# Performance work log

Measured on AMD Instinct MI355X. Metric: run time of the kernel, lower is better.

## Reference

```python
import jax, jax.numpy as jnp
import numpy as np

NUM_HEADS = 16
WINDOW = 64


def setup_inputs() -> dict:
    key = jax.random.key(0)
    ks = jax.random.split(key, 6)
    b, l, d = 2, 2048, 1024
    s = 1.0 / np.sqrt(d)
    return {
        "x": jax.random.normal(ks[0], (b, l, d), dtype=jnp.float32),
        "Wq": jax.random.normal(ks[1], (d, d), dtype=jnp.float32) * s,
        "Wk": jax.random.normal(ks[2], (d, d), dtype=jnp.float32) * s,
        "Wv": jax.random.normal(ks[3], (d, d), dtype=jnp.float32) * s,
        "Wo": jax.random.normal(ks[4], (d, d), dtype=jnp.float32) * s,
        "bo": jax.random.normal(ks[5], (d,), dtype=jnp.float32) * 0.01,
    }


def reference(x, Wq, Wk, Wv, Wo, bo):
    b, l, d = x.shape
    h, w = NUM_HEADS, WINDOW
    dh = d // h
    p = w // 2
    # Projections. Padding is zeros and proj_k/proj_v have no bias, so
    # padding-then-projecting equals projecting-then-zero-padding.
    q = (x @ Wq.T).reshape(b, l, h, dh)                     # (b,l,h,dh)
    xp = jnp.pad(x, ((0, 0), (p, p), (0, 0)))               # (b,l+2p,d)
    k = (xp @ Wk.T).reshape(b, l + 2 * p, h, dh)
    v = (xp @ Wv.T).reshape(b, l + 2 * p, h, dh)
    # Sliding windows: query i attends to padded positions i .. i+w-1
    win_idx = jnp.arange(l)[:, None] + jnp.arange(w)[None, :]  # (l,w)
    kw = k[:, win_idx]                                       # (b,l,w,h,dh)
    vw = v[:, win_idx]                                       # (b,l,w,h,dh)
    scale = 1.0 / np.float32(np.sqrt(dh))
    scores = jnp.einsum('blhd,blwhd->blhw', q, kw) * scale   # (b,l,h,w)
    attn = jax.nn.softmax(scores, axis=-1)
    out = jnp.einsum('blhw,blwhd->blhd', attn, vw).reshape(b, l, d)
    return out @ Wo.T + bo
```

## Files before the change

kernel.cpp:

```cpp
#include <hip/hip_runtime.h>
#include <hip/hip_bf16.h>
#include <cstdint>

typedef __bf16 bf16;
typedef __bf16 bf16x4 __attribute__((ext_vector_type(4)));
typedef __bf16 bf16x8 __attribute__((ext_vector_type(8)));
typedef float floatx4 __attribute__((ext_vector_type(4)));
typedef float floatx16 __attribute__((ext_vector_type(16)));

typedef __attribute__((address_space(1))) void as1_void;
typedef __attribute__((address_space(3))) void as3_void;

__device__ __forceinline__ void gld16(const void* g, void* l) {
#if __has_builtin(__builtin_amdgcn_global_load_lds)
  __builtin_amdgcn_global_load_lds((as1_void*)(uintptr_t)g, (as3_void*)l, 16, 0, 0);
#else
  *(uint4*)l = *(const uint4*)g;
#endif
}

__global__ __launch_bounds__(256) void convert_kernel(
    const float* __restrict__ x, const float* __restrict__ wq,
    const float* __restrict__ wk, const float* __restrict__ wv,
    const float* __restrict__ wo, bf16* __restrict__ xbf,
    bf16* __restrict__ wqkv, bf16* __restrict__ wob) {
  int i = blockIdx.x * 256 + threadIdx.x;
  const float* src;
  bf16* dst;
  int off;
  if (i < 1048576) {
    src = x; dst = xbf; off = i;
  } else if (i < 1310720) {
    src = wq; dst = wqkv; off = i - 1048576;
  } else if (i < 1572864) {
    src = wk; dst = wqkv + 1048576; off = i - 1310720;
  } else if (i < 1835008) {
    src = wv; dst = wqkv + 2097152; off = i - 1572864;
  } else {
    src = wo; dst = wob; off = i - 1835008;
  }
  float4 v = ((const float4*)src)[off];
  bf16x4 o;
  o[0] = (bf16)v.x; o[1] = (bf16)v.y; o[2] = (bf16)v.z; o[3] = (bf16)v.w;
  ((bf16x4*)dst)[off] = o;
}

template <int MODE, int BM, int BN>
__global__ __launch_bounds__(256) void gemm_nt(const bf16* __restrict__ A,
                                               const bf16* __restrict__ Bm,
                                               bf16* __restrict__ Cb,
                                               float* __restrict__ Cf,
                                               const float* __restrict__ bias,
                                               int M, int N, int K) {
  constexpr int WM = BM / 2, WN = BN / 2;
  constexpr int MI = WM / 32, NI = WN / 32;
  __shared__ __attribute__((aligned(16))) bf16 As[BM * 32];
  __shared__ __attribute__((aligned(16))) bf16 Bs[BN * 32];
  const int tid = threadIdx.x;
  const int lane = tid & 63;
  const int wave = tid >> 6;
  const int m32 = lane & 31;
  const int half = lane >> 5;
  const int wm = wave >> 1;
  const int wn = wave & 1;
  const int bN = blockIdx.x, bM = blockIdx.y;
  const bf16* Ab = A + (size_t)bM * BM * K;
  const bf16* Bb = Bm + (size_t)bN * BN * K;
  floatx16 acc[MI][NI] = {};
  for (int k0 = 0; k0 < K; k0 += 32) {
#pragma unroll
    for (int cc = 0; cc < BM * 4; cc += 256) {
      const int c = cc + tid;
      gld16(Ab + (size_t)(c >> 2) * K + k0 + (c & 3) * 8, &As[c * 8]);
    }
#pragma unroll
    for (int cc = 0; cc < BN * 4; cc += 256) {
      const int c = cc + tid;
      gld16(Bb + (size_t)(c >> 2) * K + k0 + (c & 3) * 8, &Bs[c * 8]);
    }
    __syncthreads();
#pragma unroll
    for (int ks = 0; ks < 2; ++ks) {
      bf16x8 af[MI], bfr[NI];
#pragma unroll
      for (int mi = 0; mi < MI; ++mi)
        af[mi] = *(const bf16x8*)&As[(wm * WM + mi * 32 + m32) * 32 + ks * 16 + half * 8];
#pragma unroll
      for (int ni = 0; ni < NI; ++ni)
        bfr[ni] = *(const bf16x8*)&Bs[(wn * WN + ni * 32 + m32) * 32 + ks * 16 + half * 8];
#pragma unroll
      for (int mi = 0; mi < MI; ++mi)
#pragma unroll
        for (int ni = 0; ni < NI; ++ni)
          acc[mi][ni] = __builtin_amdgcn_mfma_f32_32x32x16_bf16(
              af[mi], bfr[ni], acc[mi][ni], 0, 0, 0);
    }
    __syncthreads();
  }
  const int rowBase = bM * BM + wm * WM + half * 4;
  const int colBase = bN * BN + wn * WN + m32;
#pragma unroll
  for (int ni = 0; ni < NI; ++ni) {
    const int col = colBase + ni * 32;
    float badd = 0.f;
    if (MODE == 1) badd = bias[col];
#pragma unroll
    for (int mi = 0; mi < MI; ++mi)
#pragma unroll
      for (int r = 0; r < 16; ++r) {
        const int row = rowBase + mi * 32 + (r & 3) + 8 * (r >> 2);
        if (MODE == 0)
          Cb[(size_t)row * N + col] = (bf16)acc[mi][ni][r];
        else
          Cf[(size_t)row * N + col] = acc[mi][ni][r] + badd;
      }
  }
}

__global__ __launch_bounds__(256) void attn_kernel(const bf16* __restrict__ qkv,
                                                   bf16* __restrict__ aout) {
  __shared__ __attribute__((aligned(16))) bf16 Ks[128 * 72];
  __shared__ __attribute__((aligned(16))) bf16 VsPs[128 * 72];
  __shared__ __attribute__((aligned(16))) bf16 Vt[64 * 136];
  const int bid = blockIdx.x;
  const int b = bid >> 9;
  const int h = (bid >> 5) & 15;
  const int i0 = (bid & 31) * 64;
  const int tid = threadIdx.x;
  const int wave = tid >> 6, lane = tid & 63;
  const int quad = lane >> 4, n0 = lane & 15;
  bf16* Vs = VsPs;

#pragma unroll
  for (int it = 0; it < 4; ++it) {
    const int idx = it * 256 + tid;
    const int r = idx >> 3, c = idx & 7;
    const int j = i0 - 32 + r;
    uint4 kv_ = make_uint4(0u, 0u, 0u, 0u);
    uint4 vv = make_uint4(0u, 0u, 0u, 0u);
    if (j >= 0 && j < 2048) {
      const bf16* base = qkv + (size_t)(b * 2048 + j) * 3072 + 1024 + h * 64 + c * 8;
      kv_ = *(const uint4*)base;
      vv = *(const uint4*)(base + 1024);
    }
    *(uint4*)&Ks[r * 72 + c * 8] = kv_;
    *(uint4*)&Vs[r * 72 + c * 8] = vv;
  }
  __syncthreads();

#pragma unroll
  for (int it = 0; it < 4; ++it) {
    const int idx = it * 256 + tid;
    const int t = idx & 127, c = idx >> 7;
    bf16x8 v = *(const bf16x8*)&Vs[t * 72 + c * 8];
#pragma unroll
    for (int jj = 0; jj < 8; ++jj) Vt[(c * 8 + jj) * 136 + t] = v[jj];
  }
  __syncthreads();

  bf16x8 aq[2];
#pragma unroll
  for (int ks = 0; ks < 2; ++ks)
    aq[ks] = *(const bf16x8*)(qkv +
        (size_t)(b * 2048 + i0 + wave * 16 + n0) * 3072 + h * 64 + ks * 32 + quad * 8);

  floatx4 accS[8] = {};
#pragma unroll
  for (int nt = 0; nt < 8; ++nt)
#pragma unroll
    for (int ks = 0; ks < 2; ++ks) {
      bf16x8 bk = *(const bf16x8*)&Ks[(nt * 16 + n0) * 72 + ks * 32 + quad * 8];
      accS[nt] = __builtin_amdgcn_mfma_f32_16x16x32_bf16(aq[ks], bk, accS[nt], 0, 0, 0);
    }

  float mrow[4] = {-1e30f, -1e30f, -1e30f, -1e30f};
#pragma unroll
  for (int nt = 0; nt < 8; ++nt)
#pragma unroll
    for (int r = 0; r < 4; ++r) {
      const int q64 = wave * 16 + quad * 4 + r;
      const int t = nt * 16 + n0;
      float s = accS[nt][r] * 0.125f;
      if (t < q64 || t >= q64 + 64) s = -1e30f;
      accS[nt][r] = s;
      mrow[r] = fmaxf(mrow[r], s);
    }
#pragma unroll
  for (int off = 1; off < 16; off <<= 1)
#pragma unroll
    for (int r = 0; r < 4; ++r)
      mrow[r] = fmaxf(mrow[r], __shfl_xor(mrow[r], off));
  float lrow[4] = {0.f, 0.f, 0.f, 0.f};
#pragma unroll
  for (int nt = 0; nt < 8; ++nt)
#pragma unroll
    for (int r = 0; r < 4; ++r) {
      const float e = __expf(accS[nt][r] - mrow[r]);
      accS[nt][r] = e;
      lrow[r] += e;
    }
#pragma unroll
  for (int off = 1; off < 16; off <<= 1)
#pragma unroll
    for (int r = 0; r < 4; ++r) lrow[r] += __shfl_xor(lrow[r], off);

  bf16* Pw = &VsPs[wave * 16 * 136];
#pragma unroll
  for (int r = 0; r < 4; ++r) {
    const float inv = 1.f / lrow[r];
#pragma unroll
    for (int nt = 0; nt < 8; ++nt)
      Pw[(quad * 4 + r) * 136 + nt * 16 + n0] = (bf16)(accS[nt][r] * inv);
  }

  floatx4 accO[4] = {};
#pragma unroll
  for (int kt = 0; kt < 4; ++kt) {
    bf16x8 ap = *(const bf16x8*)&Pw[n0 * 136 + kt * 32 + quad * 8];
#pragma unroll
    for (int dt = 0; dt < 4; ++dt) {
      bf16x8 bv = *(const bf16x8*)&Vt[(dt * 16 + n0) * 136 + kt * 32 + quad * 8];
      accO[dt] = __builtin_amdgcn_mfma_f32_16x16x32_bf16(ap, bv, accO[dt], 0, 0, 0);
    }
  }
#pragma unroll
  for (int dt = 0; dt < 4; ++dt)
#pragma unroll
    for (int r = 0; r < 4; ++r) {
      const int q64 = wave * 16 + quad * 4 + r;
      aout[(size_t)(b * 2048 + i0 + q64) * 1024 + h * 64 + dt * 16 + n0] =
          (bf16)accO[dt][r];
    }
}

extern "C" void kernel_launch(void* const* d_in, const int* in_sizes, int n_in,
                              void* d_out, int out_size, void* d_ws, size_t ws_size,
                              hipStream_t stream) {
  const float* x = (const float*)d_in[0];
  const float* wq = (const float*)d_in[1];
  const float* wk = (const float*)d_in[2];
  const float* wv = (const float*)d_in[3];
  const float* wo = (const float*)d_in[4];
  const float* bo = (const float*)d_in[5];
  char* ws = (char*)d_ws;
  bf16* xbf = (bf16*)(ws);
  bf16* wqkv = (bf16*)(ws + (8u << 20));
  bf16* wob = (bf16*)(ws + (14u << 20));
  bf16* qkv = (bf16*)(ws + (16u << 20));
  bf16* aout = xbf;

  convert_kernel<<<8192, 256, 0, stream>>>(x, wq, wk, wv, wo, xbf, wqkv, wob);
  gemm_nt<0, 64, 128><<<dim3(24, 64), 256, 0, stream>>>(xbf, wqkv, qkv, nullptr,
                                                        nullptr, 4096, 3072, 1024);
  attn_kernel<<<1024, 256, 0, stream>>>(qkv, aout);
  gemm_nt<1, 64, 64><<<dim3(16, 64), 256, 0, stream>>>(aout, wob, nullptr,
                                                       (float*)d_out, bo, 4096,
                                                       1024, 1024);
}
```

Measured before the change: 175.9 us.

## Double-buffer GEMM tiles via register prefetch and enlarge M tile size

Replaces the direct global-to-LDS loads with register-staged prefetch of the next K-slice into a second shared-memory buffer. This overlaps global memory latency with MFMA work and drops one barrier per iteration. Both GEMMs also move to BM=128 tiles, which halves the grid and raises per-block reuse. The cost is more registers and LDS per block, which can lower occupancy, and fewer blocks (768 and 512) to spread across the CUs.

```diff
diff --git a/kernel.cpp b/kernel.cpp
--- a/kernel.cpp
+++ b/kernel.cpp
@@ -7,17 +7,6 @@
 typedef __bf16 bf16x8 __attribute__((ext_vector_type(8)));
 typedef float floatx4 __attribute__((ext_vector_type(4)));
 typedef float floatx16 __attribute__((ext_vector_type(16)));
-
-typedef __attribute__((address_space(1))) void as1_void;
-typedef __attribute__((address_space(3))) void as3_void;
-
-__device__ __forceinline__ void gld16(const void* g, void* l) {
-#if __has_builtin(__builtin_amdgcn_global_load_lds)
-  __builtin_amdgcn_global_load_lds((as1_void*)(uintptr_t)g, (as3_void*)l, 16, 0, 0);
-#else
-  *(uint4*)l = *(const uint4*)g;
-#endif
-}
 
 __global__ __launch_bounds__(256) void convert_kernel(
     const float* __restrict__ x, const float* __restrict__ wq,
@@ -54,8 +43,10 @@
                                                int M, int N, int K) {
   constexpr int WM = BM / 2, WN = BN / 2;
   constexpr int MI = WM / 32, NI = WN / 32;
-  __shared__ __attribute__((aligned(16))) bf16 As[BM * 32];
-  __shared__ __attribute__((aligned(16))) bf16 Bs[BN * 32];
+  constexpr int AC = BM * 4 / 256;
+  constexpr int BC = BN * 4 / 256;
+  __shared__ __attribute__((aligned(16))) bf16 As[2][BM * 32];
+  __shared__ __attribute__((aligned(16))) bf16 Bs[2][BN * 32];
   const int tid = threadIdx.x;
   const int lane = tid & 63;
   const int wave = tid >> 6;
@@ -67,27 +58,50 @@
   const bf16* Ab = A + (size_t)bM * BM * K;
   const bf16* Bb = Bm + (size_t)bN * BN * K;
   floatx16 acc[MI][NI] = {};
-  for (int k0 = 0; k0 < K; k0 += 32) {
-#pragma unroll
-    for (int cc = 0; cc < BM * 4; cc += 256) {
-      const int c = cc + tid;
-      gld16(Ab + (size_t)(c >> 2) * K + k0 + (c & 3) * 8, &As[c * 8]);
-    }
-#pragma unroll
-    for (int cc = 0; cc < BN * 4; cc += 256) {
-      const int c = cc + tid;
-      gld16(Bb + (size_t)(c >> 2) * K + k0 + (c & 3) * 8, &Bs[c * 8]);
-    }
-    __syncthreads();
+  const int nIter = K >> 5;
+
+  uint4 ra[AC], rb[BC];
+#pragma unroll
+  for (int j = 0; j < AC; ++j) {
+    const int c = j * 256 + tid;
+    ra[j] = *(const uint4*)(Ab + (size_t)(c >> 2) * K + (c & 3) * 8);
+  }
+#pragma unroll
+  for (int j = 0; j < BC; ++j) {
+    const int c = j * 256 + tid;
+    rb[j] = *(const uint4*)(Bb + (size_t)(c >> 2) * K + (c & 3) * 8);
+  }
+#pragma unroll
+  for (int j = 0; j < AC; ++j) *(uint4*)&As[0][(j * 256 + tid) * 8] = ra[j];
+#pragma unroll
+  for (int j = 0; j < BC; ++j) *(uint4*)&Bs[0][(j * 256 + tid) * 8] = rb[j];
+  __syncthreads();
+
+  for (int i = 0; i < nIter; ++i) {
+    const int buf = i & 1;
+    const bool more = (i + 1) < nIter;
+    const int k1 = (i + 1) << 5;
+    if (more) {
+#pragma unroll
+      for (int j = 0; j < AC; ++j) {
+        const int c = j * 256 + tid;
+        ra[j] = *(const uint4*)(Ab + (size_t)(c >> 2) * K + k1 + (c & 3) * 8);
+      }
+#pragma unroll
+      for (int j = 0; j < BC; ++j) {
+        const int c = j * 256 + tid;
+        rb[j] = *(const uint4*)(Bb + (size_t)(c >> 2) * K + k1 + (c & 3) * 8);
+      }
+    }
 #pragma unroll
     for (int ks = 0; ks < 2; ++ks) {
       bf16x8 af[MI], bfr[NI];
 #pragma unroll
       for (int mi = 0; mi < MI; ++mi)
-        af[mi] = *(const bf16x8*)&As[(wm * WM + mi * 32 + m32) * 32 + ks * 16 + half * 8];
+        af[mi] = *(const bf16x8*)&As[buf][(wm * WM + mi * 32 + m32) * 32 + ks * 16 + half * 8];
 #pragma unroll
       for (int ni = 0; ni < NI; ++ni)
-        bfr[ni] = *(const bf16x8*)&Bs[(wn * WN + ni * 32 + m32) * 32 + ks * 16 + half * 8];
+        bfr[ni] = *(const bf16x8*)&Bs[buf][(wn * WN + ni * 32 + m32) * 32 + ks * 16 + half * 8];
 #pragma unroll
       for (int mi = 0; mi < MI; ++mi)
 #pragma unroll
@@ -95,8 +109,15 @@
           acc[mi][ni] = __builtin_amdgcn_mfma_f32_32x32x16_bf16(
               af[mi], bfr[ni], acc[mi][ni], 0, 0, 0);
     }
-    __syncthreads();
-  }
+    if (more) {
+#pragma unroll
+      for (int j = 0; j < AC; ++j) *(uint4*)&As[buf ^ 1][(j * 256 + tid) * 8] = ra[j];
+#pragma unroll
+      for (int j = 0; j < BC; ++j) *(uint4*)&Bs[buf ^ 1][(j * 256 + tid) * 8] = rb[j];
+      __syncthreads();
+    }
+  }
+
   const int rowBase = bM * BM + wm * WM + half * 4;
   const int colBase = bN * BN + wn * WN + m32;
 #pragma unroll
@@ -250,10 +271,10 @@
   bf16* aout = xbf;
 
   convert_kernel<<<8192, 256, 0, stream>>>(x, wq, wk, wv, wo, xbf, wqkv, wob);
-  gemm_nt<0, 64, 128><<<dim3(24, 64), 256, 0, stream>>>(xbf, wqkv, qkv, nullptr,
-                                                        nullptr, 4096, 3072, 1024);
+  gemm_nt<0, 128, 128><<<dim3(24, 32), 256, 0, stream>>>(xbf, wqkv, qkv, nullptr,
+                                                         nullptr, 4096, 3072, 1024);
   attn_kernel<<<1024, 256, 0, stream>>>(qkv, aout);
-  gemm_nt<1, 64, 64><<<dim3(16, 64), 256, 0, stream>>>(aout, wob, nullptr,
-                                                       (float*)d_out, bo, 4096,
-                                                       1024, 1024);
-}
+  gemm_nt<1, 128, 64><<<dim3(16, 32), 256, 0, stream>>>(aout, wob, nullptr,
+                                                        (float*)d_out, bo, 4096,
+                                                        1024, 1024);
+}
```

New measurement: 256.7 us. +45.9%, slower.
